# Performance work log

Hardware: AMD Instinct MI355X
Metric: run time of the kernel (lower is better)

The kernel has to match this reference:

```python
import jax, jax.numpy as jnp
import numpy as np


def _softmax_kernel(data, proj, is_query, eps=1e-4):
    # data: [b,h,n,d], proj: [m,d] -> features [b,h,n,m]
    d = data.shape[-1]
    data_normalizer = d ** -0.25
    ratio = proj.shape[0] ** -0.5
    data_dash = jnp.einsum('bhnd,md->bhnm', data_normalizer * data, proj)
    diag_data = jnp.sum(data * data, axis=-1, keepdims=True) * 0.5 * (data_normalizer ** 2)
    if is_query:
        stab = jnp.max(data_dash, axis=-1, keepdims=True)
    else:
        stab = jnp.max(data_dash, axis=(-1, -2), keepdims=True)
    stab = jax.lax.stop_gradient(stab)
    return ratio * (jnp.exp(data_dash - diag_data - stab) + eps)


def setup_inputs() -> dict:
    key = jax.random.key(0)
    k1, k2, k3, k4 = jax.random.split(key, 4)
    b, h, n, d, m = 8, 16, 4096, 64, 256
    q = jax.random.normal(k1, (b, h, n, d), dtype=jnp.float32)
    k = jax.random.normal(k2, (b, h, n, d), dtype=jnp.float32)
    v = jax.random.normal(k3, (b, h, n, d), dtype=jnp.float32)
    projection_matrix = jax.random.normal(k4, (m, d), dtype=jnp.float32)
    return {'q': q, 'k': k, 'v': v, 'projection_matrix': projection_matrix}


def reference(q, k, v, projection_matrix):
    # FAVOR+ softmax-kernel features
    q_prime = _softmax_kernel(q, projection_matrix, is_query=True)   # [b,h,n,m]
    k_prime = _softmax_kernel(k, projection_matrix, is_query=False)  # [b,h,n,m]
    # Non-causal linear attention
    k_sum = jnp.sum(k_prime, axis=-2)                                # [b,h,m]
    d_inv = 1.0 / jnp.einsum('bhnm,bhm->bhn', q_prime, k_sum)        # [b,h,n]
    context = jnp.einsum('bhnm,bhne->bhme', k_prime, v)              # [b,h,m,e]
    out = jnp.einsum('bhme,bhnm,bhn->bhne', context, q_prime, d_inv) # [b,h,n,e]
    return out
```

## Files before the change

### kernel.cpp

```cpp
#include <hip/hip_runtime.h>


#define BH 128
#define NN 4096
#define DD 64
#define MM 256
#define NORM 0.35355339059327373f
#define EPS 1e-4f

typedef unsigned short u16;
typedef __attribute__((ext_vector_type(8))) short bfrag;
typedef __attribute__((ext_vector_type(4))) float ffrag;
#define MFMA16(A,B,C) __builtin_amdgcn_mfma_f32_16x16x32_bf16(A,B,C,0,0,0)

__device__ __forceinline__ float u2f(u16 h){ return __uint_as_float(((unsigned)h)<<16); }
__device__ __forceinline__ void splitf(float x, u16 &h, u16 &l){
    unsigned uh = __float_as_uint(x) & 0xffff0000u;
    h = (u16)(uh >> 16);
    float r = x - __uint_as_float(uh);
    l = (u16)(__float_as_uint(r) >> 16);
}

__global__ void p0_proj(const float* __restrict__ proj, u16* __restrict__ phi, u16* __restrict__ plo){
    int idx = blockIdx.x*256 + threadIdx.x;
    u16 h,l; splitf(proj[idx], h, l);
    phi[idx] = h; plo[idx] = l;
}

__global__ __launch_bounds__(256) void p0_vt(const float* __restrict__ vin,
        u16* __restrict__ vthi, u16* __restrict__ vtlo, float* __restrict__ vsum){
    int head = blockIdx.x >> 6;
    int n0 = (blockIdx.x & 63) * 64;
    int t = threadIdx.x;
    __shared__ float tile[64][65];
    {
        int row = t >> 2, c0 = (t & 3) * 16;
        const float* src = vin + ((size_t)head*NN + n0 + row)*64 + c0;
        #pragma unroll
        for (int i=0;i<4;++i){
            float4 x = *(const float4*)(src + i*4);
            tile[row][c0+i*4+0]=x.x; tile[row][c0+i*4+1]=x.y;
            tile[row][c0+i*4+2]=x.z; tile[row][c0+i*4+3]=x.w;
        }
    }
    __syncthreads();
    {
        int e = t >> 2, nq = (t & 3) * 16;
        float s = 0.f;
        unsigned ph[8], pl[8];
        #pragma unroll
        for (int jj=0;jj<8;++jj){
            float x0 = tile[nq+jj*2+0][e];
            float x1 = tile[nq+jj*2+1][e];
            s += x0 + x1;
            u16 h0,l0,h1,l1; splitf(x0,h0,l0); splitf(x1,h1,l1);
            ph[jj] = (unsigned)h0 | ((unsigned)h1<<16);
            pl[jj] = (unsigned)l0 | ((unsigned)l1<<16);
        }
        size_t base = ((size_t)head*64 + e)*NN + n0 + nq;
        uint4 a0; a0.x=ph[0]; a0.y=ph[1]; a0.z=ph[2]; a0.w=ph[3];
        uint4 a1; a1.x=ph[4]; a1.y=ph[5]; a1.z=ph[6]; a1.w=ph[7];
        uint4 b0; b0.x=pl[0]; b0.y=pl[1]; b0.z=pl[2]; b0.w=pl[3];
        uint4 b1; b1.x=pl[4]; b1.y=pl[5]; b1.z=pl[6]; b1.w=pl[7];
        *(uint4*)(vthi + base)     = a0;
        *(uint4*)(vthi + base + 8) = a1;
        *(uint4*)(vtlo + base)     = b0;
        *(uint4*)(vtlo + base + 8) = b1;
        s += __shfl_xor(s, 1);
        s += __shfl_xor(s, 2);
        if ((t & 3) == 0) atomicAdd(vsum + head*64 + e, s);
    }
}

__global__ __launch_bounds__(256,2) void kc_kernel(
        const float* __restrict__ kin, const u16* __restrict__ phi, const u16* __restrict__ plo,
        const u16* __restrict__ vthi, const u16* __restrict__ vtlo,
        float* __restrict__ ctxPart, float* __restrict__ mbArr)
{
    const int blk  = blockIdx.x;
    const int head = blk >> 3;
    const int n0   = (blk & 7) * 512;
    const int t    = threadIdx.x;
    const int w    = t >> 6;
    const int lane = t & 63;
    const int qd   = lane >> 4;
    const int li   = lane & 15;

    __shared__ __attribute__((aligned(16))) u16 knh[32*64], knl[32*64];
    __shared__ __attribute__((aligned(16))) u16 bsh[256*32], bsl[256*32];
    __shared__ float diag_s[32];
    __shared__ float wmax[4];

    bfrag pf[4][2][2];
    #pragma unroll
    for (int mt=0;mt<4;++mt){
        int m = w*64 + mt*16 + li;
        #pragma unroll
        for (int ks=0;ks<2;++ks){
            pf[mt][ks][0] = *(const bfrag*)(phi + m*64 + ks*32 + qd*8);
            pf[mt][ks][1] = *(const bfrag*)(plo + m*64 + ks*32 + qd*8);
        }
    }

    ffrag acc[4][4];
    #pragma unroll
    for (int et=0;et<4;++et)
        #pragma unroll
        for (int mt=0;mt<4;++mt){ ffrag z = {0.f,0.f,0.f,0.f}; acc[et][mt] = z; }
    float ks[4] = {0.f,0.f,0.f,0.f};
    float M = -3.0e38f;

    const float* kg = kin + ((size_t)head*NN + n0)*64;

    for (int sub=0; sub<16; ++sub){
        {
            int row = t >> 3;
            int g   = t & 7;
            const float* src = kg + (size_t)(sub*32 + row)*64 + g*8;
            float4 x0 = *(const float4*)(src);
            float4 x1 = *(const float4*)(src + 4);
            float xs[8] = {x0.x,x0.y,x0.z,x0.w,x1.x,x1.y,x1.z,x1.w};
            bfrag hv, lv;
            float ss = 0.f;
            #pragma unroll
            for (int j=0;j<8;++j){
                float xn = xs[j]*NORM;
                ss += xn*xn;
                u16 hh,ll; splitf(xn,hh,ll);
                hv[j] = (short)hh; lv[j] = (short)ll;
            }
            int gs = g ^ (row & 7);
            *(bfrag*)(knh + row*64 + gs*8) = hv;
            *(bfrag*)(knl + row*64 + gs*8) = lv;
            ss += __shfl_xor(ss, 1);
            ss += __shfl_xor(ss, 2);
            ss += __shfl_xor(ss, 4);
            if ((t & 7) == 0) diag_s[row] = 0.5f*ss;
        }
        __syncthreads();

        ffrag d1[2][4];
        #pragma unroll
        for (int nt=0;nt<2;++nt)
            #pragma unroll
            for (int mt=0;mt<4;++mt){ ffrag z = {0.f,0.f,0.f,0.f}; d1[nt][mt] = z; }
        #pragma unroll
        for (int nt=0;nt<2;++nt){
            int n = nt*16 + li;
            bfrag ah[2], al[2];
            #pragma unroll
            for (int kss=0;kss<2;++kss){
                int gp = (kss*4 + qd) ^ (n & 7);
                ah[kss] = *(const bfrag*)(knh + n*64 + gp*8);
                al[kss] = *(const bfrag*)(knl + n*64 + gp*8);
            }
            #pragma unroll
            for (int mt=0;mt<4;++mt){
                #pragma unroll
                for (int kss=0;kss<2;++kss){
                    d1[nt][mt] = MFMA16(ah[kss], pf[mt][kss][0], d1[nt][mt]);
                    d1[nt][mt] = MFMA16(ah[kss], pf[mt][kss][1], d1[nt][mt]);
                    d1[nt][mt] = MFMA16(al[kss], pf[mt][kss][0], d1[nt][mt]);
                }
            }
        }

        float mx = -3.0e38f;
        #pragma unroll
        for (int nt=0;nt<2;++nt)
            #pragma unroll
            for (int mt=0;mt<4;++mt)
                #pragma unroll
                for (int rg=0;rg<4;++rg) mx = fmaxf(mx, d1[nt][mt][rg]);
        mx = fmaxf(mx, __shfl_xor(mx, 1));
        mx = fmaxf(mx, __shfl_xor(mx, 2));
        mx = fmaxf(mx, __shfl_xor(mx, 4));
        mx = fmaxf(mx, __shfl_xor(mx, 8));
        mx = fmaxf(mx, __shfl_xor(mx, 16));
        mx = fmaxf(mx, __shfl_xor(mx, 32));
        if (lane == 0) wmax[w] = mx;
        __syncthreads();
        float Ms = fmaxf(fmaxf(wmax[0],wmax[1]), fmaxf(wmax[2],wmax[3]));
        float Mn = fmaxf(M, Ms);
        float r  = __expf(M - Mn);
        M = Mn;
        #pragma unroll
        for (int mt=0;mt<4;++mt) ks[mt] *= r;
        #pragma unroll
        for (int et=0;et<4;++et)
            #pragma unroll
            for (int mt=0;mt<4;++mt)
                #pragma unroll
                for (int rg=0;rg<4;++rg) acc[et][mt][rg] *= r;

        float sl[4] = {0.f,0.f,0.f,0.f};
        #pragma unroll
        for (int nt=0;nt<2;++nt){
            float d4[4];
            #pragma unroll
            for (int rg=0;rg<4;++rg) d4[rg] = diag_s[nt*16 + qd*4 + rg];
            #pragma unroll
            for (int mt=0;mt<4;++mt){
                int m = w*64 + mt*16 + li;
                u16 h4[4], l4[4];
                #pragma unroll
                for (int rg=0;rg<4;++rg){
                    float f = __expf(d1[nt][mt][rg] - d4[rg] - M);
                    sl[mt] += f;
                    splitf(f, h4[rg], l4[rg]);
                }
                int g  = nt*2 + (qd>>1);
                int gp = g ^ ((m>>1)&3);
                int off = m*32 + gp*8 + (qd&1)*4;
                *(ushort4*)(bsh + off) = make_ushort4(h4[0],h4[1],h4[2],h4[3]);
                *(ushort4*)(bsl + off) = make_ushort4(l4[0],l4[1],l4[2],l4[3]);
            }
        }
        #pragma unroll
        for (int mt=0;mt<4;++mt){
            float v = sl[mt];
            v += __shfl_xor(v, 16);
            v += __shfl_xor(v, 32);
            ks[mt] += v;
        }
        __syncthreads();

        bfrag bh[4], bl[4];
        #pragma unroll
        for (int mt=0;mt<4;++mt){
            int m = w*64 + mt*16 + li;
            int gp = qd ^ ((m>>1)&3);
            bh[mt] = *(const bfrag*)(bsh + m*32 + gp*8);
            bl[mt] = *(const bfrag*)(bsl + m*32 + gp*8);
        }
        #pragma unroll
        for (int et=0;et<4;++et){
            int e = et*16 + li;
            size_t vb = ((size_t)head*64 + e)*NN + n0 + sub*32 + qd*8;
            bfrag avh = *(const bfrag*)(vthi + vb);
            bfrag avl = *(const bfrag*)(vtlo + vb);
            #pragma unroll
            for (int mt=0;mt<4;++mt){
                acc[et][mt] = MFMA16(avh, bh[mt], acc[et][mt]);
                acc[et][mt] = MFMA16(avh, bl[mt], acc[et][mt]);
                acc[et][mt] = MFMA16(avl, bh[mt], acc[et][mt]);
            }
        }
        __syncthreads();
    }

    float* P = ctxPart + (size_t)blk * (65*256);
    #pragma unroll
    for (int et=0;et<4;++et)
        #pragma unroll
        for (int mt=0;mt<4;++mt)
            #pragma unroll
            for (int rg=0;rg<4;++rg){
                int e = et*16 + qd*4 + rg;
                int m = w*64 + mt*16 + li;
                P[e*256 + m] = acc[et][mt][rg];
            }
    if (qd == 0){
        #pragma unroll
        for (int mt=0;mt<4;++mt) P[64*256 + w*64 + mt*16 + li] = ks[mt];
    }
    if (t == 0) mbArr[blk] = M;
}

__global__ __launch_bounds__(256) void kred(const float* __restrict__ ctxPart,
        const float* __restrict__ mbArr, const float* __restrict__ vsum,
        u16* __restrict__ ctxh, u16* __restrict__ ctxl, float* __restrict__ ksumG){
    int head = blockIdx.x / 65;
    int e = blockIdx.x % 65;
    int m = threadIdx.x;
    float mb[8];
    float mk = -3.0e38f;
    #pragma unroll
    for (int c=0;c<8;++c){ mb[c] = mbArr[head*8+c]; mk = fmaxf(mk, mb[c]); }
    float s = 0.f;
    #pragma unroll
    for (int c=0;c<8;++c){
        float sc = __expf(mb[c] - mk);
        s += sc * ctxPart[((size_t)(head*8+c)*65 + e)*256 + m];
    }
    if (e == 64){
        ksumG[head*256 + m] = s + 4096.0f*EPS;
    } else {
        float val = s + EPS * vsum[head*64 + e];
        u16 h,l; splitf(val,h,l);
        ctxh[((size_t)head*64 + e)*256 + m] = h;
        ctxl[((size_t)head*64 + e)*256 + m] = l;
    }
}

__global__ __launch_bounds__(256,2) void k3_kernel(
        const float* __restrict__ qin, const u16* __restrict__ phi, const u16* __restrict__ plo,
        const u16* __restrict__ ctxh, const u16* __restrict__ ctxl,
        const float* __restrict__ ksumG, float* __restrict__ out)
{
    const int head = blockIdx.x >> 6;
    const int n0   = (blockIdx.x & 63) * 64;
    const int t    = threadIdx.x;
    const int w    = t >> 6;
    const int lane = t & 63;
    const int qd   = lane >> 4;
    const int li   = lane & 15;

    __shared__ __attribute__((aligned(16))) u16 SM[32768];
    u16* qnh = SM;
    u16* qnl = SM + 4096;
    u16* fh  = SM;
    u16* fl  = SM + 16384;
    __shared__ float diagq[64], drm[64], dinvs[64], ksums[256], wred[256];

    ksums[t] = ksumG[head*256 + t];
    {
        int row = t >> 2;
        const float* src = qin + ((size_t)head*NN + n0 + row)*64 + (t&3)*16;
        float ss = 0.f;
        #pragma unroll
        for (int gi=0; gi<2; ++gi){
            int g = (t&3)*2 + gi;
            float4 x0 = *(const float4*)(src + gi*8);
            float4 x1 = *(const float4*)(src + gi*8 + 4);
            float xs[8] = {x0.x,x0.y,x0.z,x0.w,x1.x,x1.y,x1.z,x1.w};
            bfrag hv, lv;
            #pragma unroll
            for (int j=0;j<8;++j){
                float xn = xs[j]*NORM;
                ss += xn*xn;
                u16 hh,ll; splitf(xn,hh,ll);
                hv[j] = (short)hh; lv[j] = (short)ll;
            }
            int gs = g ^ (row & 7);
            *(bfrag*)(qnh + row*64 + gs*8) = hv;
            *(bfrag*)(qnl + row*64 + gs*8) = lv;
        }
        ss += __shfl_xor(ss, 1);
        ss += __shfl_xor(ss, 2);
        if ((t&3) == 0) diagq[row] = 0.5f*ss;
    }

    bfrag pf[4][2][2];
    #pragma unroll
    for (int mt=0;mt<4;++mt){
        int m = w*64 + mt*16 + li;
        #pragma unroll
        for (int kss=0;kss<2;++kss){
            pf[mt][kss][0] = *(const bfrag*)(phi + m*64 + kss*32 + qd*8);
            pf[mt][kss][1] = *(const bfrag*)(plo + m*64 + kss*32 + qd*8);
        }
    }
    __syncthreads();

    ffrag d1[4][4];
    #pragma unroll
    for (int nt=0;nt<4;++nt)
        #pragma unroll
        for (int mt=0;mt<4;++mt){ ffrag z = {0.f,0.f,0.f,0.f}; d1[nt][mt] = z; }
    #pragma unroll
    for (int nt=0;nt<4;++nt){
        int n = nt*16 + li;
        bfrag ah[2], al[2];
        #pragma unroll
        for (int kss=0;kss<2;++kss){
            int gp = (kss*4 + qd) ^ (n & 7);
            ah[kss] = *(const bfrag*)(qnh + n*64 + gp*8);
            al[kss] = *(const bfrag*)(qnl + n*64 + gp*8);
        }
        #pragma unroll
        for (int mt=0;mt<4;++mt){
            #pragma unroll
            for (int kss=0;kss<2;++kss){
                d1[nt][mt] = MFMA16(ah[kss], pf[mt][kss][0], d1[nt][mt]);
                d1[nt][mt] = MFMA16(ah[kss], pf[mt][kss][1], d1[nt][mt]);
                d1[nt][mt] = MFMA16(al[kss], pf[mt][kss][0], d1[nt][mt]);
            }
        }
    }

    #pragma unroll
    for (int nt=0;nt<4;++nt){
        #pragma unroll
        for (int rg=0;rg<4;++rg){
            float v = fmaxf(fmaxf(d1[nt][0][rg], d1[nt][1][rg]),
                            fmaxf(d1[nt][2][rg], d1[nt][3][rg]));
            v = fmaxf(v, __shfl_xor(v, 1));
            v = fmaxf(v, __shfl_xor(v, 2));
            v = fmaxf(v, __shfl_xor(v, 4));
            v = fmaxf(v, __shfl_xor(v, 8));
            if (li == 0) wred[w*64 + nt*16 + qd*4 + rg] = v;
        }
    }
    __syncthreads();
    if (t < 64){
        float rm = fmaxf(fmaxf(wred[t], wred[64+t]), fmaxf(wred[128+t], wred[192+t]));
        drm[t] = diagq[t] + rm;
    }
    __syncthreads();

    #pragma unroll
    for (int nt=0;nt<4;++nt){
        float dr4[4];
        #pragma unroll
        for (int rg=0;rg<4;++rg) dr4[rg] = drm[nt*16 + qd*4 + rg];
        #pragma unroll
        for (int mt=0;mt<4;++mt){
            int m = w*64 + mt*16 + li;
            #pragma unroll
            for (int rg=0;rg<4;++rg){
                int n = nt*16 + qd*4 + rg;
                float f = __expf(d1[nt][mt][rg] - dr4[rg]) + EPS;
                u16 hh,ll; splitf(f,hh,ll);
                int idx = n*256 + (((m>>3) ^ (n&7))*8) + (m&7);
                fh[idx] = hh; fl[idx] = ll;
            }
        }
    }
    __syncthreads();

    {
        int row = t >> 2, seg = t & 3;
        float s = 0.f;
        #pragma unroll
        for (int g=0; g<8; ++g){
            int gl = seg*8 + g;
            int gp = gl ^ (row & 7);
            bfrag hvv = *(const bfrag*)(fh + row*256 + gp*8);
            bfrag lvv = *(const bfrag*)(fl + row*256 + gp*8);
            #pragma unroll
            for (int j=0;j<8;++j){
                float f = u2f((u16)hvv[j]) + u2f((u16)lvv[j]);
                s += f * ksums[gl*8 + j];
            }
        }
        wred[t] = s;
    }
    __syncthreads();
    if (t < 64){
        float dsum = wred[4*t] + wred[4*t+1] + wred[4*t+2] + wred[4*t+3];
        dinvs[t] = 1.0f / dsum;
    }
    __syncthreads();

    ffrag a2[4];
    #pragma unroll
    for (int et=0;et<4;++et){ ffrag z = {0.f,0.f,0.f,0.f}; a2[et] = z; }
    const u16* cbh = ctxh + (size_t)head*64*256;
    const u16* cbl = ctxl + (size_t)head*64*256;
    int n2 = w*16 + li;
    #pragma unroll
    for (int ksm=0; ksm<8; ++ksm){
        int gp = (ksm*4 + qd) ^ (n2 & 7);
        bfrag ah2 = *(const bfrag*)(fh + n2*256 + gp*8);
        bfrag al2 = *(const bfrag*)(fl + n2*256 + gp*8);
        #pragma unroll
        for (int et=0;et<4;++et){
            int e = et*16 + li;
            bfrag ch = *(const bfrag*)(cbh + e*256 + ksm*32 + qd*8);
            bfrag cl = *(const bfrag*)(cbl + e*256 + ksm*32 + qd*8);
            a2[et] = MFMA16(ah2, ch, a2[et]);
            a2[et] = MFMA16(ah2, cl, a2[et]);
            a2[et] = MFMA16(al2, ch, a2[et]);
        }
    }

    float dvr[4];
    #pragma unroll
    for (int rg=0;rg<4;++rg) dvr[rg] = dinvs[w*16 + qd*4 + rg];
    float* og = out + ((size_t)head*NN + n0 + w*16)*64;
    #pragma unroll
    for (int et=0;et<4;++et)
        #pragma unroll
        for (int rg=0;rg<4;++rg)
            og[(qd*4+rg)*64 + et*16 + li] = a2[et][rg] * dvr[rg];
}

extern "C" void kernel_launch(void* const* d_in, const int* in_sizes, int n_in,
                              void* d_out, int out_size, void* d_ws, size_t ws_size,
                              hipStream_t stream) {
    const float* q    = (const float*)d_in[0];
    const float* k    = (const float*)d_in[1];
    const float* v    = (const float*)d_in[2];
    const float* proj = (const float*)d_in[3];
    float* out = (float*)d_out;

    char* wp = (char*)d_ws;
    u16* phi     = (u16*)wp;  wp += (size_t)MM*DD*2;
    u16* plo     = (u16*)wp;  wp += (size_t)MM*DD*2;
    u16* vthi    = (u16*)wp;  wp += (size_t)BH*64*NN*2;
    u16* vtlo    = (u16*)wp;  wp += (size_t)BH*64*NN*2;
    float* vsum  = (float*)wp; wp += (size_t)BH*64*4;
    float* mbArr = (float*)wp; wp += (size_t)1024*4;
    float* ctxPart = (float*)wp; wp += (size_t)1024*65*256*4;
    u16* ctxh    = (u16*)wp;  wp += (size_t)BH*64*256*2;
    u16* ctxl    = (u16*)wp;  wp += (size_t)BH*64*256*2;
    float* ksumG = (float*)wp; wp += (size_t)BH*256*4;

    hipMemsetAsync(vsum, 0, (size_t)BH*64*4, stream);
    p0_proj<<<64, 256, 0, stream>>>(proj, phi, plo);
    p0_vt<<<BH*64, 256, 0, stream>>>(v, vthi, vtlo, vsum);
    kc_kernel<<<1024, 256, 0, stream>>>(k, phi, plo, vthi, vtlo, ctxPart, mbArr);
    kred<<<BH*65, 256, 0, stream>>>(ctxPart, mbArr, vsum, ctxh, ctxl, ksumG);
    k3_kernel<<<BH*64, 256, 0, stream>>>(q, phi, plo, ctxh, ctxl, ksumG, out);
}
```

Baseline: 876.2 us.

## Restructure k3 MFMA operand roles and fuse denominator into feature write

The query-side kernel now puts the projection as the A operand and the query as B, so row maxima come from cross-quad shuffles and feature tiles are written as ushort4 vectors instead of scalar u16 stores. The ksum dot product is fused into the exp pass using per-lane register ksum values, which removes the separate shared-memory readback pass and one barrier. The second GEMM swaps roles so each wave owns an e-tile and loads its context fragment once per k-step. The block index is remapped so neighbouring blocks cover different heads, and launch bounds become waves_per_eu(2,2). In exchange, output stores change to a strided pattern and register pressure may shift.

```diff
diff --git a/kernel.cpp b/kernel.cpp
--- a/kernel.cpp
+++ b/kernel.cpp
@@ -72,7 +72,8 @@
     }
 }
 
-__global__ __launch_bounds__(256,2) void kc_kernel(
+__global__ __launch_bounds__(256) __attribute__((amdgpu_waves_per_eu(2,2)))
+void kc_kernel(
         const float* __restrict__ kin, const u16* __restrict__ phi, const u16* __restrict__ plo,
         const u16* __restrict__ vthi, const u16* __restrict__ vtlo,
         float* __restrict__ ctxPart, float* __restrict__ mbArr)
@@ -293,13 +294,15 @@
     }
 }
 
-__global__ __launch_bounds__(256,2) void k3_kernel(
+__global__ __launch_bounds__(256) __attribute__((amdgpu_waves_per_eu(2,2)))
+void k3_kernel(
         const float* __restrict__ qin, const u16* __restrict__ phi, const u16* __restrict__ plo,
         const u16* __restrict__ ctxh, const u16* __restrict__ ctxl,
         const float* __restrict__ ksumG, float* __restrict__ out)
 {
-    const int head = blockIdx.x >> 6;
-    const int n0   = (blockIdx.x & 63) * 64;
+    const int bx   = blockIdx.x;
+    const int head = (bx & 7) + 8 * ((bx >> 3) & 15);
+    const int n0   = (bx >> 7) * 64;
     const int t    = threadIdx.x;
     const int w    = t >> 6;
     const int lane = t & 63;
@@ -311,9 +314,8 @@
     u16* qnl = SM + 4096;
     u16* fh  = SM;
     u16* fl  = SM + 16384;
-    __shared__ float diagq[64], drm[64], dinvs[64], ksums[256], wred[256];
-
-    ksums[t] = ksumG[head*256 + t];
+    __shared__ float diagq[64], drm[64], dinvs[64], wm[4][64];
+
     {
         int row = t >> 2;
         const float* src = qin + ((size_t)head*NN + n0 + row)*64 + (t&3)*16;
@@ -341,139 +343,121 @@
         if ((t&3) == 0) diagq[row] = 0.5f*ss;
     }
 
-    bfrag pf[4][2][2];
-    #pragma unroll
-    for (int mt=0;mt<4;++mt){
-        int m = w*64 + mt*16 + li;
-        #pragma unroll
-        for (int kss=0;kss<2;++kss){
-            pf[mt][kss][0] = *(const bfrag*)(phi + m*64 + kss*32 + qd*8);
-            pf[mt][kss][1] = *(const bfrag*)(plo + m*64 + kss*32 + qd*8);
-        }
-    }
+    float4 ks4[4];
+    #pragma unroll
+    for (int mt=0;mt<4;++mt)
+        ks4[mt] = *(const float4*)(ksumG + head*256 + w*64 + mt*16 + qd*4);
     __syncthreads();
 
     ffrag d1[4][4];
     #pragma unroll
-    for (int nt=0;nt<4;++nt)
-        #pragma unroll
-        for (int mt=0;mt<4;++mt){ ffrag z = {0.f,0.f,0.f,0.f}; d1[nt][mt] = z; }
+    for (int mt=0;mt<4;++mt)
+        #pragma unroll
+        for (int nt=0;nt<4;++nt){ ffrag z = {0.f,0.f,0.f,0.f}; d1[mt][nt] = z; }
+    #pragma unroll
+    for (int kss=0;kss<2;++kss){
+        bfrag pfh[4], pfl[4];
+        #pragma unroll
+        for (int mt=0;mt<4;++mt){
+            int m = w*64 + mt*16 + li;
+            pfh[mt] = *(const bfrag*)(phi + m*64 + kss*32 + qd*8);
+            pfl[mt] = *(const bfrag*)(plo + m*64 + kss*32 + qd*8);
+        }
+        #pragma unroll
+        for (int nt=0;nt<4;++nt){
+            int n = nt*16 + li;
+            int gp = (kss*4 + qd) ^ (n & 7);
+            bfrag bh = *(const bfrag*)(qnh + n*64 + gp*8);
+            bfrag bl = *(const bfrag*)(qnl + n*64 + gp*8);
+            #pragma unroll
+            for (int mt=0;mt<4;++mt){
+                d1[mt][nt] = MFMA16(pfh[mt], bh, d1[mt][nt]);
+                d1[mt][nt] = MFMA16(pfh[mt], bl, d1[mt][nt]);
+                d1[mt][nt] = MFMA16(pfl[mt], bh, d1[mt][nt]);
+            }
+        }
+    }
+
+    #pragma unroll
+    for (int nt=0;nt<4;++nt){
+        float mx = -3.0e38f;
+        #pragma unroll
+        for (int mt=0;mt<4;++mt)
+            #pragma unroll
+            for (int rg=0;rg<4;++rg) mx = fmaxf(mx, d1[mt][nt][rg]);
+        mx = fmaxf(mx, __shfl_xor(mx, 16));
+        mx = fmaxf(mx, __shfl_xor(mx, 32));
+        if (qd == 0) wm[w][nt*16 + li] = mx;
+    }
+    __syncthreads();
+    if (t < 64)
+        drm[t] = diagq[t] + fmaxf(fmaxf(wm[0][t], wm[1][t]), fmaxf(wm[2][t], wm[3][t]));
+    __syncthreads();
+
+    float ds[4] = {0.f,0.f,0.f,0.f};
     #pragma unroll
     for (int nt=0;nt<4;++nt){
         int n = nt*16 + li;
-        bfrag ah[2], al[2];
-        #pragma unroll
-        for (int kss=0;kss<2;++kss){
-            int gp = (kss*4 + qd) ^ (n & 7);
-            ah[kss] = *(const bfrag*)(qnh + n*64 + gp*8);
-            al[kss] = *(const bfrag*)(qnl + n*64 + gp*8);
-        }
+        float dr = drm[n];
         #pragma unroll
         for (int mt=0;mt<4;++mt){
-            #pragma unroll
-            for (int kss=0;kss<2;++kss){
-                d1[nt][mt] = MFMA16(ah[kss], pf[mt][kss][0], d1[nt][mt]);
-                d1[nt][mt] = MFMA16(ah[kss], pf[mt][kss][1], d1[nt][mt]);
-                d1[nt][mt] = MFMA16(al[kss], pf[mt][kss][0], d1[nt][mt]);
-            }
-        }
-    }
-
+            float fv[4];
+            u16 h4[4], l4[4];
+            #pragma unroll
+            for (int rg=0;rg<4;++rg){
+                fv[rg] = __expf(d1[mt][nt][rg] - dr) + EPS;
+                splitf(fv[rg], h4[rg], l4[rg]);
+            }
+            ds[nt] += fv[0]*ks4[mt].x + fv[1]*ks4[mt].y + fv[2]*ks4[mt].z + fv[3]*ks4[mt].w;
+            int G  = w*8 + mt*2 + (qd>>1);
+            int Gp = G ^ (li & 7);
+            int off = n*256 + Gp*8 + (qd&1)*4;
+            *(ushort4*)(fh + off) = make_ushort4(h4[0],h4[1],h4[2],h4[3]);
+            *(ushort4*)(fl + off) = make_ushort4(l4[0],l4[1],l4[2],l4[3]);
+        }
+    }
     #pragma unroll
     for (int nt=0;nt<4;++nt){
+        float v = ds[nt];
+        v += __shfl_xor(v, 16);
+        v += __shfl_xor(v, 32);
+        if (qd == 0) wm[w][nt*16 + li] = v;
+    }
+    __syncthreads();
+    if (t < 64)
+        dinvs[t] = 1.0f / (wm[0][t] + wm[1][t] + wm[2][t] + wm[3][t]);
+    __syncthreads();
+
+    ffrag a2[4];
+    #pragma unroll
+    for (int nt=0;nt<4;++nt){ ffrag z = {0.f,0.f,0.f,0.f}; a2[nt] = z; }
+    const u16* cbh = ctxh + (size_t)head*64*256 + (w*16 + li)*256;
+    const u16* cbl = ctxl + (size_t)head*64*256 + (w*16 + li)*256;
+    #pragma unroll
+    for (int ksm=0; ksm<8; ++ksm){
+        bfrag ch = *(const bfrag*)(cbh + ksm*32 + qd*8);
+        bfrag cl = *(const bfrag*)(cbl + ksm*32 + qd*8);
+        #pragma unroll
+        for (int nt=0;nt<4;++nt){
+            int n = nt*16 + li;
+            int Gp = (ksm*4 + qd) ^ (li & 7);
+            bfrag ah2 = *(const bfrag*)(fh + n*256 + Gp*8);
+            bfrag al2 = *(const bfrag*)(fl + n*256 + Gp*8);
+            a2[nt] = MFMA16(ah2, ch, a2[nt]);
+            a2[nt] = MFMA16(ah2, cl, a2[nt]);
+            a2[nt] = MFMA16(al2, ch, a2[nt]);
+        }
+    }
+
+    float* og = out + ((size_t)head*NN + n0)*64;
+    #pragma unroll
+    for (int nt=0;nt<4;++nt){
         #pragma unroll
         for (int rg=0;rg<4;++rg){
-            float v = fmaxf(fmaxf(d1[nt][0][rg], d1[nt][1][rg]),
-                            fmaxf(d1[nt][2][rg], d1[nt][3][rg]));
-            v = fmaxf(v, __shfl_xor(v, 1));
-            v = fmaxf(v, __shfl_xor(v, 2));
-            v = fmaxf(v, __shfl_xor(v, 4));
-            v = fmaxf(v, __shfl_xor(v, 8));
-            if (li == 0) wred[w*64 + nt*16 + qd*4 + rg] = v;
-        }
-    }
-    __syncthreads();
-    if (t < 64){
-        float rm = fmaxf(fmaxf(wred[t], wred[64+t]), fmaxf(wred[128+t], wred[192+t]));
-        drm[t] = diagq[t] + rm;
-    }
-    __syncthreads();
-
-    #pragma unroll
-    for (int nt=0;nt<4;++nt){
-        float dr4[4];
-        #pragma unroll
-        for (int rg=0;rg<4;++rg) dr4[rg] = drm[nt*16 + qd*4 + rg];
-        #pragma unroll
-        for (int mt=0;mt<4;++mt){
-            int m = w*64 + mt*16 + li;
-            #pragma unroll
-            for (int rg=0;rg<4;++rg){
-                int n = nt*16 + qd*4 + rg;
-                float f = __expf(d1[nt][mt][rg] - dr4[rg]) + EPS;
-                u16 hh,ll; splitf(f,hh,ll);
-                int idx = n*256 + (((m>>3) ^ (n&7))*8) + (m&7);
-                fh[idx] = hh; fl[idx] = ll;
-            }
-        }
-    }
-    __syncthreads();
-
-    {
-        int row = t >> 2, seg = t & 3;
-        float s = 0.f;
-        #pragma unroll
-        for (int g=0; g<8; ++g){
-            int gl = seg*8 + g;
-            int gp = gl ^ (row & 7);
-            bfrag hvv = *(const bfrag*)(fh + row*256 + gp*8);
-            bfrag lvv = *(const bfrag*)(fl + row*256 + gp*8);
-            #pragma unroll
-            for (int j=0;j<8;++j){
-                float f = u2f((u16)hvv[j]) + u2f((u16)lvv[j]);
-                s += f * ksums[gl*8 + j];
-            }
-        }
-        wred[t] = s;
-    }
-    __syncthreads();
-    if (t < 64){
-        float dsum = wred[4*t] + wred[4*t+1] + wred[4*t+2] + wred[4*t+3];
-        dinvs[t] = 1.0f / dsum;
-    }
-    __syncthreads();
-
-    ffrag a2[4];
-    #pragma unroll
-    for (int et=0;et<4;++et){ ffrag z = {0.f,0.f,0.f,0.f}; a2[et] = z; }
-    const u16* cbh = ctxh + (size_t)head*64*256;
-    const u16* cbl = ctxl + (size_t)head*64*256;
-    int n2 = w*16 + li;
-    #pragma unroll
-    for (int ksm=0; ksm<8; ++ksm){
-        int gp = (ksm*4 + qd) ^ (n2 & 7);
-        bfrag ah2 = *(const bfrag*)(fh + n2*256 + gp*8);
-        bfrag al2 = *(const bfrag*)(fl + n2*256 + gp*8);
-        #pragma unroll
-        for (int et=0;et<4;++et){
-            int e = et*16 + li;
-            bfrag ch = *(const bfrag*)(cbh + e*256 + ksm*32 + qd*8);
-            bfrag cl = *(const bfrag*)(cbl + e*256 + ksm*32 + qd*8);
-            a2[et] = MFMA16(ah2, ch, a2[et]);
-            a2[et] = MFMA16(ah2, cl, a2[et]);
-            a2[et] = MFMA16(al2, ch, a2[et]);
-        }
-    }
-
-    float dvr[4];
-    #pragma unroll
-    for (int rg=0;rg<4;++rg) dvr[rg] = dinvs[w*16 + qd*4 + rg];
-    float* og = out + ((size_t)head*NN + n0 + w*16)*64;
-    #pragma unroll
-    for (int et=0;et<4;++et)
-        #pragma unroll
-        for (int rg=0;rg<4;++rg)
-            og[(qd*4+rg)*64 + et*16 + li] = a2[et][rg] * dvr[rg];
+            int n = nt*16 + qd*4 + rg;
+            og[(size_t)n*64 + w*16 + li] = a2[nt][rg] * dinvs[n];
+        }
+    }
 }
 
 extern "C" void kernel_launch(void* const* d_in, const int* in_sizes, int n_in,
```

Measured after the change: 705.9 us. -19.4%, faster.
